# Kernel optimization log

Measured on AMD Instinct MI355X. Metric: run time of the kernel, lower is better.

The kernel has to match this reference:

```python
import jax, jax.numpy as jnp
import numpy as np

HEADS = 16
DIM_HEAD = 32
WSZ = 7
DIM = 512
INNER = HEADS * DIM_HEAD
LN_EPS = 1e-5


def setup_inputs() -> dict:
    key = jax.random.key(0)
    ks = jax.random.split(key, 9)
    b, H, W = 16, 56, 56
    x = jax.random.normal(ks[0], (b, DIM, H, W), dtype=jnp.float32)
    w_qkv = jax.random.normal(ks[1], (INNER * 3, DIM), dtype=jnp.float32) * (DIM ** -0.5)
    window_tokens = jax.random.normal(ks[2], (DIM,), dtype=jnp.float32)
    ln_w = jnp.ones((DIM_HEAD,), dtype=jnp.float32)
    ln_b = jnp.zeros((DIM_HEAD,), dtype=jnp.float32)
    w_qk = jax.random.normal(ks[3], (INNER * 2, INNER), dtype=jnp.float32) * (INNER ** -0.5)
    b_qk = jnp.zeros((INNER * 2,), dtype=jnp.float32)
    w_out = jax.random.normal(ks[4], (DIM, INNER), dtype=jnp.float32) * (INNER ** -0.5)
    b_out = jnp.zeros((DIM,), dtype=jnp.float32)
    return {"x": x, "w_qkv": w_qkv, "window_tokens": window_tokens,
            "ln_w": ln_w, "ln_b": ln_b, "w_qk": w_qk, "b_qk": b_qk,
            "w_out": w_out, "b_out": b_out}


def reference(x, w_qkv, window_tokens, ln_w, ln_b, w_qk, b_qk, w_out, b_out):
    b, c, H, W = x.shape
    h, d, wsz = HEADS, DIM_HEAD, WSZ
    X, Y = H // wsz, W // wsz
    nw = X * Y            # number of windows per image
    n = wsz * wsz         # tokens per window (49)
    scale = d ** -0.5

    # b c (X w1) (Y w2) -> (b X Y) c (w1 w2)
    xw = x.reshape(b, c, X, wsz, Y, wsz).transpose(0, 2, 4, 1, 3, 5).reshape(b * nw, c, n)
    wt = jnp.broadcast_to(window_tokens[None, :, None], (b * nw, c, 1))
    xc = jnp.concatenate([wt, xw], axis=-1)                 # [BW, c, n+1]

    qkv = jnp.einsum('oc,bcn->bon', w_qkv, xc)              # 1x1 conv, no bias
    q, k, v = jnp.split(qkv, 3, axis=1)
    def to_heads(t):
        return t.reshape(t.shape[0], h, d, n + 1).transpose(0, 1, 3, 2)  # [BW,h,n+1,d]
    q, k, v = to_heads(q), to_heads(k), to_heads(v)

    dots = jnp.einsum('bhid,bhjd->bhij', q * scale, k)      # [BW,h,50,50]
    attn = jax.nn.softmax(dots, axis=-1)
    out = jnp.einsum('bhij,bhjd->bhid', attn, v)            # [BW,h,50,d]

    wtok = out[:, :, 0].reshape(b, nw, h, d).transpose(0, 2, 1, 3)          # [b,h,nw,d]
    wfm = out[:, :, 1:].reshape(b, nw, h, n, d).transpose(0, 2, 1, 3, 4)    # [b,h,nw,n,d]

    # window_tokens_to_qk: LayerNorm(d) -> GELU -> conv1d(inner, 2*inner)
    mu = wtok.mean(-1, keepdims=True)
    var = wtok.var(-1, keepdims=True)
    normed = (wtok - mu) / jnp.sqrt(var + LN_EPS) * ln_w + ln_b
    g = jax.nn.gelu(normed, approximate=False)
    gf = g.transpose(0, 1, 3, 2).reshape(b, h * d, nw)      # b h n c -> b (h c) n
    qk = jnp.einsum('oc,bcn->bon', w_qk, gf) + b_qk[None, :, None]
    qk = qk.reshape(b, h, 2 * d, nw).transpose(0, 1, 3, 2)  # [b,h,nw,2d]
    w_q, w_k = qk[..., :d], qk[..., d:]

    w_dots = jnp.einsum('bhid,bhjd->bhij', w_q * scale, w_k)  # [b,h,nw,nw]
    w_attn = jax.nn.softmax(w_dots, axis=-1)
    agg = jnp.einsum('bhij,bhjnd->bhind', w_attn, wfm)        # [b,h,nw,n,d]

    # b h (X Y) (w1 w2) d -> b (h d) (X w1) (Y w2)
    fmap = agg.reshape(b, h, X, Y, wsz, wsz, d).transpose(0, 1, 6, 2, 4, 3, 5).reshape(b, h * d, H, W)
    return jnp.einsum('oc,bchw->bohw', w_out, fmap) + b_out[None, :, None, None]
```

## Files before the change

### kernel.cpp

```cpp
#include <hip/hip_runtime.h>
#include <math.h>

#define SCALE_D 0.17677669529663687f

typedef __attribute__((ext_vector_type(8))) short short8;
typedef __attribute__((ext_vector_type(4))) float f32x4;

__device__ __forceinline__ unsigned short f2bf(float f) {
  unsigned u = __builtin_bit_cast(unsigned, f);
  unsigned r = u + 0x7FFF + ((u >> 16) & 1);
  return (unsigned short)(r >> 16);
}
__device__ __forceinline__ float bf2f(unsigned short h) {
  unsigned u = ((unsigned)h) << 16;
  return __builtin_bit_cast(float, u);
}
__device__ __forceinline__ void gload16(const void* g, void* l) {
  __builtin_amdgcn_global_load_lds((const __attribute__((address_space(1))) unsigned int*)g,
                                   (__attribute__((address_space(3))) unsigned int*)l,
                                   16, 0, 0);
}

__global__ __launch_bounds__(256) void k_split(const float* __restrict__ src,
                                               unsigned short* __restrict__ hi,
                                               unsigned short* __restrict__ lo, int n) {
  int i = blockIdx.x * 256 + threadIdx.x;
  if (i < n) {
    float v = src[i];
    unsigned short h = f2bf(v);
    hi[i] = h;
    lo[i] = f2bf(v - bf2f(h));
  }
}

__global__ __launch_bounds__(256) void k_build_xcT(const float* __restrict__ x,
                                                   const float* __restrict__ wtok,
                                                   unsigned short* __restrict__ Thi,
                                                   unsigned short* __restrict__ Tlo,
                                                   int bb0) {
  const int cblk = blockIdx.x;
  const int h    = blockIdx.y;
  const int bbL  = blockIdx.z;
  const int bb   = bb0 + bbL;
  const int tid  = threadIdx.x;
  const int c0   = cblk * 64;
  if (h == 56) {
    for (int e = tid; e < 4096; e += 256) {
      int wl = e >> 6, cl = e & 63;
      float v = wtok[c0 + cl];
      unsigned short hv = f2bf(v);
      long idx = ((long)(bbL * 64 + wl) * 50) * 512 + c0 + cl;
      Thi[idx] = hv;
      Tlo[idx] = f2bf(v - bf2f(hv));
    }
    return;
  }
  __shared__ unsigned short shi[64][57], slo[64][57];
  const int Xw = h / 7, r7 = h % 7;
  for (int e = tid; e < 3584; e += 256) {
    int cl = e / 56, w = e - cl * 56;
    float v = x[((long)(bb * 512 + c0 + cl) * 56 + h) * 56 + w];
    unsigned short hv = f2bf(v);
    shi[cl][w] = hv;
    slo[cl][w] = f2bf(v - bf2f(hv));
  }
  __syncthreads();
  for (int e = tid; e < 3584; e += 256) {
    int row = e >> 6, cl = e & 63;
    int Yw = row / 7, c7 = row - Yw * 7;
    long trow = (long)(bbL * 64 + Xw * 8 + Yw) * 50 + 1 + r7 * 7 + c7;
    Thi[trow * 512 + c0 + cl] = shi[cl][row];
    Tlo[trow * 512 + c0 + cl] = slo[cl][row];
  }
}

template <int PACK>
__global__ __launch_bounds__(256, 2) void k_gemm_mfma(
    const unsigned short* __restrict__ Ahi, const unsigned short* __restrict__ Alo,
    const unsigned short* __restrict__ Bhi, const unsigned short* __restrict__ Blo,
    float* __restrict__ C, const float* __restrict__ bias,
    int NC, int brow_stride, long c_stride) {
  __shared__ unsigned short lds[2][4][128][32];
  const int tid = threadIdx.x;
  const int wv = tid >> 6, lane = tid & 63;

  const int gy = gridDim.y;
  const int nwg = gridDim.x * gy;
  int hw = blockIdx.y * gridDim.x + blockIdx.x;
  int flat;
  {
    int q = nwg >> 3, r = nwg & 7;
    int xcd = hw & 7, k = hw >> 3;
    int start = (xcd < r) ? xcd * (q + 1) : r * (q + 1) + (xcd - r) * q;
    flat = start + k;
  }
  const int bx = flat / gy, by = flat % gy;
  const int m0 = by * 128, n0 = bx * 128;
  const long brow0 = (long)blockIdx.z * brow_stride + n0;
  C += (long)blockIdx.z * c_stride;

  const int wr = wv >> 1, wc = wv & 1;
  const int lr = lane & 15, kb = lane >> 4;
  const int srow = lane >> 2, sju = lane & 3;
  const int sswz = (sju ^ ((srow >> 1) & 3)) * 8;
  const int rswz = (lr >> 1) & 3;

  f32x4 acc[4][4];
#pragma unroll
  for (int i = 0; i < 4; ++i)
#pragma unroll
    for (int j = 0; j < 4; ++j) {
      f32x4 z = {0.f, 0.f, 0.f, 0.f};
      acc[i][j] = z;
    }

  auto STAGE = [&](int buf, int k0) {
#pragma unroll
    for (int it = 0; it < 2; ++it) {
      const int rloc = (wv * 2 + it) * 16;
      const int r = rloc + srow;
      const long ga = (long)(m0 + r) * 512 + k0 + sswz;
      gload16(Ahi + ga, &lds[buf][0][rloc][0]);
      gload16(Alo + ga, &lds[buf][1][rloc][0]);
      const long gb = (brow0 + r) * 512 + k0 + sswz;
      gload16(Bhi + gb, &lds[buf][2][rloc][0]);
      gload16(Blo + gb, &lds[buf][3][rloc][0]);
    }
  };

  STAGE(0, 0);
  int cur = 0;
  for (int t = 0; t < 16; ++t) {
    if (t < 15) STAGE(cur ^ 1, (t + 1) * 32);
    if (t < 15) {
      asm volatile("s_waitcnt vmcnt(8)" ::: "memory");
    } else {
      asm volatile("s_waitcnt vmcnt(0)" ::: "memory");
    }
    __builtin_amdgcn_s_barrier();
    asm volatile("" ::: "memory");
    short8 ah[4], al[4], bh[4], bl[4];
#pragma unroll
    for (int f = 0; f < 4; ++f) {
      int ra = wr * 64 + f * 16 + lr;
      int ca = (kb ^ rswz) * 8;
      ah[f] = *(const short8*)&lds[cur][0][ra][ca];
      al[f] = *(const short8*)&lds[cur][1][ra][ca];
      int rb = wc * 64 + f * 16 + lr;
      bh[f] = *(const short8*)&lds[cur][2][rb][ca];
      bl[f] = *(const short8*)&lds[cur][3][rb][ca];
    }
#pragma unroll
    for (int i = 0; i < 4; ++i)
#pragma unroll
      for (int j = 0; j < 4; ++j) {
        acc[i][j] = __builtin_amdgcn_mfma_f32_16x16x32_bf16(ah[i], bh[j], acc[i][j], 0, 0, 0);
        acc[i][j] = __builtin_amdgcn_mfma_f32_16x16x32_bf16(ah[i], bl[j], acc[i][j], 0, 0, 0);
        acc[i][j] = __builtin_amdgcn_mfma_f32_16x16x32_bf16(al[i], bh[j], acc[i][j], 0, 0, 0);
      }
    asm volatile("s_waitcnt lgkmcnt(0)" ::: "memory");
    __builtin_amdgcn_s_barrier();
    asm volatile("" ::: "memory");
    cur ^= 1;
  }

#pragma unroll
  for (int i = 0; i < 4; ++i)
#pragma unroll
    for (int nf = 0; nf < 4; ++nf) {
      int col = n0 + wc * 64 + nf * 16 + lr;
      if (col < NC) {
#pragma unroll
        for (int j4 = 0; j4 < 4; ++j4) {
          int row = m0 + wr * 64 + i * 16 + kb * 4 + j4;
          float v = acc[i][nf][j4];
          if (PACK) {
            unsigned short h = f2bf(v);
            unsigned short l = f2bf(v - bf2f(h));
            ((unsigned*)C)[(long)row * NC + col] = (unsigned)h | ((unsigned)l << 16);
          } else {
            C[(long)row * NC + col] = v + (bias ? bias[row] : 0.f);
          }
        }
      }
    }
}

__global__ __launch_bounds__(256) void k_attn1_mfma(const unsigned* __restrict__ QKV,
                                                    float* __restrict__ OUT1, int w0) {
  __shared__ unsigned short P[4][16][72];
  const int tid = threadIdx.x;
  const int wv = tid >> 6, lane = tid & 63;
  const int idx = blockIdx.x * 4 + wv;
  const int wl = idx >> 4, h = idx & 15;
  const int lr = lane & 15, kb = lane >> 4;
  const long tb = (long)wl * 50;

  short8 kh[4], kl[4];
#pragma unroll
  for (int jt = 0; jt < 4; ++jt) {
#pragma unroll
    for (int e = 0; e < 8; ++e) {
      unsigned u = QKV[(long)(512 + h * 32 + kb * 8 + e) * 12800 + tb + jt * 16 + lr];
      kh[jt][e] = (short)(u & 0xFFFF);
      kl[jt][e] = (short)(u >> 16);
    }
  }
  short8 vh[2][2], vl[2][2];
#pragma unroll
  for (int ddt = 0; ddt < 2; ++ddt)
#pragma unroll
    for (int ks = 0; ks < 2; ++ks) {
      const long vb = (long)(1024 + h * 32 + ddt * 16 + lr) * 12800 + tb + ks * 32 + kb * 8;
#pragma unroll
      for (int e = 0; e < 8; ++e) {
        int j = ks * 32 + kb * 8 + e;
        unsigned u = (j < 50) ? QKV[vb + e] : 0u;
        vh[ddt][ks][e] = (short)(u & 0xFFFF);
        vl[ddt][ks][e] = (short)(u >> 16);
      }
    }

  const long ob = (long)((w0 + wl) * 16 + h) * 1600;

  for (int it = 0; it < 4; ++it) {
    short8 qh, ql;
#pragma unroll
    for (int e = 0; e < 8; ++e) {
      unsigned u = QKV[(long)(h * 32 + kb * 8 + e) * 12800 + tb + it * 16 + lr];
      qh[e] = (short)(u & 0xFFFF);
      ql[e] = (short)(u >> 16);
    }
    f32x4 s[4];
#pragma unroll
    for (int jt = 0; jt < 4; ++jt) {
      f32x4 z = {0.f, 0.f, 0.f, 0.f};
      s[jt] = z;
      s[jt] = __builtin_amdgcn_mfma_f32_16x16x32_bf16(qh, kh[jt], s[jt], 0, 0, 0);
      s[jt] = __builtin_amdgcn_mfma_f32_16x16x32_bf16(qh, kl[jt], s[jt], 0, 0, 0);
      s[jt] = __builtin_amdgcn_mfma_f32_16x16x32_bf16(ql, kh[jt], s[jt], 0, 0, 0);
#pragma unroll
      for (int r = 0; r < 4; ++r) s[jt][r] *= SCALE_D;
    }
    if (lr >= 2) {
#pragma unroll
      for (int r = 0; r < 4; ++r) s[3][r] = -1e30f;
    }
    float ex[4][4], rinv[4];
#pragma unroll
    for (int r = 0; r < 4; ++r) {
      float m = fmaxf(fmaxf(s[0][r], s[1][r]), fmaxf(s[2][r], s[3][r]));
      m = fmaxf(m, __shfl_xor(m, 1));
      m = fmaxf(m, __shfl_xor(m, 2));
      m = fmaxf(m, __shfl_xor(m, 4));
      m = fmaxf(m, __shfl_xor(m, 8));
      float sm = 0.f;
#pragma unroll
      for (int jt = 0; jt < 4; ++jt) {
        ex[jt][r] = __expf(s[jt][r] - m);
        sm += ex[jt][r];
      }
      sm += __shfl_xor(sm, 1);
      sm += __shfl_xor(sm, 2);
      sm += __shfl_xor(sm, 4);
      sm += __shfl_xor(sm, 8);
      rinv[r] = 1.f / sm;
    }
#pragma unroll
    for (int jt = 0; jt < 4; ++jt)
#pragma unroll
      for (int r = 0; r < 4; ++r)
        P[wv][kb * 4 + r][jt * 16 + lr] = f2bf(ex[jt][r] * rinv[r]);
    short8 pa0 = *(const short8*)&P[wv][lr][kb * 8];
    short8 pa1 = *(const short8*)&P[wv][lr][32 + kb * 8];
    f32x4 o[2];
#pragma unroll
    for (int ddt = 0; ddt < 2; ++ddt) {
      f32x4 z = {0.f, 0.f, 0.f, 0.f};
      o[ddt] = z;
      o[ddt] = __builtin_amdgcn_mfma_f32_16x16x32_bf16(pa0, vh[ddt][0], o[ddt], 0, 0, 0);
      o[ddt] = __builtin_amdgcn_mfma_f32_16x16x32_bf16(pa0, vl[ddt][0], o[ddt], 0, 0, 0);
      o[ddt] = __builtin_amdgcn_mfma_f32_16x16x32_bf16(pa1, vh[ddt][1], o[ddt], 0, 0, 0);
      o[ddt] = __builtin_amdgcn_mfma_f32_16x16x32_bf16(pa1, vl[ddt][1], o[ddt], 0, 0, 0);
    }
#pragma unroll
    for (int ddt = 0; ddt < 2; ++ddt)
#pragma unroll
      for (int r = 0; r < 4; ++r) {
        int i = it * 16 + kb * 4 + r;
        if (i < 50) OUT1[ob + i * 32 + ddt * 16 + lr] = o[ddt][r];
      }
  }
}

__global__ __launch_bounds__(256) void k_gemm(const float* __restrict__ A,
                                              const float* __restrict__ Bg,
                                              float* __restrict__ C,
                                              const float* __restrict__ bias,
                                              int M, int N, int K, long sB, long sC) {
  Bg += (long)blockIdx.z * sB;
  C  += (long)blockIdx.z * sC;
  __shared__ __align__(16) float As[32][132];
  __shared__ __align__(16) float Bs[32][132];
  const int tid = threadIdx.x;
  const int tx = tid & 15, ty = tid >> 4;
  const int m0 = blockIdx.y * 128, n0 = blockIdx.x * 128;

  float acc[8][8];
#pragma unroll
  for (int q = 0; q < 8; ++q)
#pragma unroll
    for (int r = 0; r < 8; ++r) acc[q][r] = 0.f;

  for (int k0 = 0; k0 < K; k0 += 32) {
#pragma unroll
    for (int it = 0; it < 4; ++it) {
      int idx = tid + it * 256;
      int row = idx >> 3, c4 = idx & 7;
      const float4 f = *(const float4*)&A[(long)(m0 + row) * K + k0 + c4 * 4];
      As[c4 * 4 + 0][row] = f.x;
      As[c4 * 4 + 1][row] = f.y;
      As[c4 * 4 + 2][row] = f.z;
      As[c4 * 4 + 3][row] = f.w;
    }
#pragma unroll
    for (int it = 0; it < 4; ++it) {
      int idx = tid + it * 256;
      int row = idx >> 5, c4 = idx & 31;
      int col = n0 + c4 * 4;
      float4 f;
      if (col + 3 < N) {
        f = *(const float4*)&Bg[(long)(k0 + row) * N + col];
      } else {
        f.x = (col + 0 < N) ? Bg[(long)(k0 + row) * N + col + 0] : 0.f;
        f.y = (col + 1 < N) ? Bg[(long)(k0 + row) * N + col + 1] : 0.f;
        f.z = (col + 2 < N) ? Bg[(long)(k0 + row) * N + col + 2] : 0.f;
        f.w = (col + 3 < N) ? Bg[(long)(k0 + row) * N + col + 3] : 0.f;
      }
      *(float4*)&Bs[row][c4 * 4] = f;
    }
    __syncthreads();
#pragma unroll
    for (int kk = 0; kk < 32; ++kk) {
      const float4 a0 = *(const float4*)&As[kk][ty * 8];
      const float4 a1 = *(const float4*)&As[kk][ty * 8 + 4];
      const float4 b0 = *(const float4*)&Bs[kk][tx * 8];
      const float4 b1 = *(const float4*)&Bs[kk][tx * 8 + 4];
      const float am[8] = {a0.x, a0.y, a0.z, a0.w, a1.x, a1.y, a1.z, a1.w};
      const float bn[8] = {b0.x, b0.y, b0.z, b0.w, b1.x, b1.y, b1.z, b1.w};
#pragma unroll
      for (int q = 0; q < 8; ++q)
#pragma unroll
        for (int r = 0; r < 8; ++r) acc[q][r] += am[q] * bn[r];
    }
    __syncthreads();
  }

#pragma unroll
  for (int q = 0; q < 8; ++q) {
    int m = m0 + ty * 8 + q;
    float bv = bias ? bias[m] : 0.f;
#pragma unroll
    for (int half = 0; half < 8; half += 4) {
      int col = n0 + tx * 8 + half;
#pragma unroll
      for (int rr = 0; rr < 4; ++rr)
        if (col + rr < N) C[(long)m * N + col + rr] = acc[q][half + rr] + bv;
    }
  }
}

__global__ __launch_bounds__(256) void k_ln_gelu(const float* __restrict__ OUT1,
                                                 const float* __restrict__ lnw,
                                                 const float* __restrict__ lnb,
                                                 float* __restrict__ G) {
  const int tid = threadIdx.x;
  const int r = blockIdx.x * 8 + (tid >> 5);
  const int l = tid & 31;
  const int bb = r >> 10, hh = (r >> 6) & 15, wp = r & 63;
  float v = OUT1[((long)((bb * 64 + wp) * 16 + hh)) * 1600 + l];
  float s = v, s2 = v * v;
#pragma unroll
  for (int o = 16; o >= 1; o >>= 1) {
    s += __shfl_xor(s, o, 32);
    s2 += __shfl_xor(s2, o, 32);
  }
  float mu = s * (1.f / 32.f);
  float var = s2 * (1.f / 32.f) - mu * mu;
  float xn = (v - mu) * rsqrtf(var + 1e-5f) * lnw[l] + lnb[l];
  float g = 0.5f * xn * (1.f + erff(xn * 0.70710678118654752f));
  G[((long)(bb * 512 + hh * 32 + l)) * 64 + wp] = g;
}

__global__ __launch_bounds__(256) void k_attn2_mfma(const float* __restrict__ QK,
                                                    const float* __restrict__ OUT1,
                                                    float* __restrict__ AGG) {
  const int bh = blockIdx.x;
  const int bb = bh >> 4, hh = bh & 15;
  const int tid = threadIdx.x;
  const int wv = tid >> 6, lane = tid & 63;
  const int lr = lane & 15, kb = lane >> 4;
  const int wr = wv >> 1, wc = wv & 1;

  __shared__ float wqs[64 * 33], wks[64 * 33];
  __shared__ float sd[64 * 65];
  __shared__ float smx[64], ssum[64];
  __shared__ __align__(16) unsigned short PAh[64][72], PAl[64][72];
  __shared__ __align__(16) unsigned short VTh[64][72], VTl[64][72];

  for (int t = tid; t < 2048; t += 256) {
    int dd = t >> 6, i = t & 63;
    wqs[i * 33 + dd] = QK[((long)(bb * 1024 + hh * 64 + dd)) * 64 + i] * SCALE_D;
    wks[i * 33 + dd] = QK[((long)(bb * 1024 + hh * 64 + 32 + dd)) * 64 + i];
  }
  __syncthreads();
  for (int t = tid; t < 4096; t += 256) {
    int i = t >> 6, j = t & 63;
    float s = 0.f;
#pragma unroll
    for (int dd = 0; dd < 32; ++dd) s += wqs[i * 33 + dd] * wks[j * 33 + dd];
    sd[i * 65 + j] = s;
  }
  __syncthreads();
  if (tid < 64) {
    float mx = -1e30f;
    for (int j = 0; j < 64; ++j) mx = fmaxf(mx, sd[tid * 65 + j]);
    float sm = 0.f;
    for (int j = 0; j < 64; ++j) sm += expf(sd[tid * 65 + j] - mx);
    smx[tid] = mx;
    ssum[tid] = 1.f / sm;
  }
  __syncthreads();
  for (int t = tid; t < 4096; t += 256) {
    int i = t >> 6, j = t & 63;
    float p = expf(sd[i * 65 + j] - smx[i]) * ssum[i];
    unsigned short h = f2bf(p);
    PAh[i][j] = h;
    PAl[i][j] = f2bf(p - bf2f(h));
  }
  __syncthreads();

  const int jstart = blockIdx.y * 13;
  const int ntiles = (blockIdx.y == 0) ? 13 : 12;
  const int swp = tid >> 2, sq = tid & 3;
  const long vbase = ((long)((bb * 64 + swp) * 16 + hh)) * 1600 + 32;
  const long abase = (long)bh * 100352;

  for (int tt = 0; tt < ntiles; ++tt) {
    const int jt = jstart + tt;
    const int jd0 = jt * 64;
    const int JT = (jt == 24) ? 32 : 64;
    for (int jj = 0; jj < (JT >> 4); ++jj) {
      const float4 v4 = *(const float4*)&OUT1[vbase + jd0 + jj * 16 + sq * 4];
#pragma unroll
      for (int e = 0; e < 4; ++e) {
        int jl = jj * 16 + sq * 4 + e;
        float v = (e == 0) ? v4.x : (e == 1) ? v4.y : (e == 2) ? v4.z : v4.w;
        unsigned short h = f2bf(v);
        VTh[jl][swp] = h;
        VTl[jl][swp] = f2bf(v - bf2f(h));
      }
    }
    __syncthreads();
#pragma unroll
    for (int mt = 0; mt < 2; ++mt) {
      const int i0 = wr * 32 + mt * 16;
#pragma unroll
      for (int nt = 0; nt < 2; ++nt) {
        const int jl0 = wc * 32 + nt * 16;
        if (jl0 < JT) {
          f32x4 acc = {0.f, 0.f, 0.f, 0.f};
#pragma unroll
          for (int ks = 0; ks < 2; ++ks) {
            const short8 pah = *(const short8*)&PAh[i0 + lr][ks * 32 + kb * 8];
            const short8 pal = *(const short8*)&PAl[i0 + lr][ks * 32 + kb * 8];
            const short8 vth = *(const short8*)&VTh[jl0 + lr][ks * 32 + kb * 8];
            const short8 vtl = *(const short8*)&VTl[jl0 + lr][ks * 32 + kb * 8];
            acc = __builtin_amdgcn_mfma_f32_16x16x32_bf16(pah, vth, acc, 0, 0, 0);
            acc = __builtin_amdgcn_mfma_f32_16x16x32_bf16(pah, vtl, acc, 0, 0, 0);
            acc = __builtin_amdgcn_mfma_f32_16x16x32_bf16(pal, vth, acc, 0, 0, 0);
          }
#pragma unroll
          for (int r = 0; r < 4; ++r)
            AGG[abase + (long)(i0 + kb * 4 + r) * 1568 + jd0 + jl0 + lr] = acc[r];
        }
      }
    }
    __syncthreads();
  }
}

__global__ __launch_bounds__(256) void k_fmap_T(const float* __restrict__ AGG,
                                                unsigned short* __restrict__ Thi,
                                                unsigned short* __restrict__ Tlo) {
  const int wp = blockIdx.x, bb = blockIdx.y;
  const int Xw = wp >> 3, Yw = wp & 7;
  const int c = threadIdx.x * 2;
  const int hh = c >> 5, d0 = c & 31;
  const long abase = ((long)(bb * 16 + hh) * 64 + wp) * 1568;
  for (int j = 0; j < 49; ++j) {
    float v0 = AGG[abase + j * 32 + d0];
    float v1 = AGG[abase + j * 32 + d0 + 1];
    int hw = (Xw * 7 + j / 7) * 56 + Yw * 7 + j % 7;
    long t = ((long)bb * 3200 + hw) * 512 + c;
    unsigned short h0 = f2bf(v0), h1 = f2bf(v1);
    unsigned short l0 = f2bf(v0 - bf2f(h0)), l1 = f2bf(v1 - bf2f(h1));
    *(unsigned*)&Thi[t] = (unsigned)h0 | ((unsigned)h1 << 16);
    *(unsigned*)&Tlo[t] = (unsigned)l0 | ((unsigned)l1 << 16);
  }
}

__global__ __launch_bounds__(256) void k_padzero(unsigned short* __restrict__ Thi,
                                                 unsigned short* __restrict__ Tlo) {
  const int bb = blockIdx.x;
  for (int e = threadIdx.x; e < 32768; e += 256) {
    long idx = ((long)bb * 3200 + 3136) * 512 + e;
    Thi[idx] = 0;
    Tlo[idx] = 0;
  }
}

extern "C" void kernel_launch(void* const* d_in, const int* in_sizes, int n_in,
                              void* d_out, int out_size, void* d_ws, size_t ws_size,
                              hipStream_t stream) {
  const float* x     = (const float*)d_in[0];
  const float* w_qkv = (const float*)d_in[1];
  const float* wt    = (const float*)d_in[2];
  const float* lnw   = (const float*)d_in[3];
  const float* lnb   = (const float*)d_in[4];
  const float* w_qk  = (const float*)d_in[5];
  const float* b_qk  = (const float*)d_in[6];
  const float* w_out = (const float*)d_in[7];
  const float* b_out = (const float*)d_in[8];
  float* out = (float*)d_out;
  float* ws  = (float*)d_ws;

  float* OUT1 = ws;
  float* AUX  = ws + 26214400L;
  unsigned short* XThi = (unsigned short*)(ws + 21233664L);
  unsigned short* XTlo = XThi + 6553600L;
  float* G  = AUX;
  float* QK = AUX + 524288L;
  unsigned short* WOhi = (unsigned short*)AUX;
  unsigned short* WOlo = WOhi + 262144L;
  unsigned short* FThi = (unsigned short*)ws;
  unsigned short* FTlo = FThi + 26214400L;

  unsigned* QKVc = (unsigned*)d_out;
  unsigned short* Whi = (unsigned short*)(out + 19660800L);
  unsigned short* Wlo = Whi + 786432L;
  float* AGG = out;

  k_split<<<3072, 256, 0, stream>>>(w_qkv, Whi, Wlo, 786432);
  for (int c = 0; c < 4; ++c) {
    k_build_xcT<<<dim3(8, 57, 4), 256, 0, stream>>>(x, wt, XThi, XTlo, c * 4);
    k_gemm_mfma<1><<<dim3(100, 12, 1), 256, 0, stream>>>(Whi, Wlo, XThi, XTlo,
                                                         (float*)QKVc, nullptr,
                                                         12800, 0, 0);
    k_attn1_mfma<<<1024, 256, 0, stream>>>(QKVc, OUT1, c * 256);
  }
  k_ln_gelu<<<2048, 256, 0, stream>>>(OUT1, lnw, lnb, G);
  k_gemm<<<dim3(1, 8, 16), 256, 0, stream>>>(w_qk, G, QK, b_qk,
                                             1024, 64, 512, 512L * 64, 1024L * 64);
  k_split<<<1024, 256, 0, stream>>>(w_out, WOhi, WOlo, 262144);
  k_attn2_mfma<<<dim3(256, 2, 1), 256, 0, stream>>>(QK, OUT1, AGG);
  k_fmap_T<<<dim3(64, 16), 256, 0, stream>>>(AGG, FThi, FTlo);
  k_padzero<<<16, 256, 0, stream>>>(FThi, FTlo);
  k_gemm_mfma<0><<<dim3(25, 4, 16), 256, 0, stream>>>(WOhi, WOlo, FThi, FTlo, out,
                                                      b_out, 3136, 3200, 512L * 3136);
}
```

Measured before the change: 788.9 us.

## Load GEMM A operand directly into double-buffered registers, stage only B in LDS

The split-bf16 MFMA GEMM now reads its A tiles (hi and lo) straight from global memory into two alternating register sets. Only the B tiles still go through LDS via global_load_lds. This halves LDS footprint and LDS read traffic per iteration. The loop is unrolled by two so the register buffers can ping-pong, with vmcnt waits adjusted to the new count of outstanding loads. In exchange it adds more VGPRs and direct global loads with per-lane row strides, which may coalesce worse than the staged path and depend on cache hits.

```diff
diff --git a/kernel.cpp b/kernel.cpp
--- a/kernel.cpp
+++ b/kernel.cpp
@@ -80,7 +80,7 @@
     const unsigned short* __restrict__ Bhi, const unsigned short* __restrict__ Blo,
     float* __restrict__ C, const float* __restrict__ bias,
     int NC, int brow_stride, long c_stride) {
-  __shared__ unsigned short lds[2][4][128][32];
+  __shared__ unsigned short lds[2][2][128][32];
   const int tid = threadIdx.x;
   const int wv = tid >> 6, lane = tid & 63;
 
@@ -104,6 +104,7 @@
   const int srow = lane >> 2, sju = lane & 3;
   const int sswz = (sju ^ ((srow >> 1) & 3)) * 8;
   const int rswz = (lr >> 1) & 3;
+  const long arow = (long)(m0 + wr * 64 + lr) * 512 + kb * 8;
 
   f32x4 acc[4][4];
 #pragma unroll
@@ -114,55 +115,85 @@
       acc[i][j] = z;
     }
 
-  auto STAGE = [&](int buf, int k0) {
+  auto STAGE_B = [&](int buf, int k0) {
 #pragma unroll
     for (int it = 0; it < 2; ++it) {
       const int rloc = (wv * 2 + it) * 16;
-      const int r = rloc + srow;
-      const long ga = (long)(m0 + r) * 512 + k0 + sswz;
-      gload16(Ahi + ga, &lds[buf][0][rloc][0]);
-      gload16(Alo + ga, &lds[buf][1][rloc][0]);
-      const long gb = (brow0 + r) * 512 + k0 + sswz;
-      gload16(Bhi + gb, &lds[buf][2][rloc][0]);
-      gload16(Blo + gb, &lds[buf][3][rloc][0]);
+      const long gb = (brow0 + rloc + srow) * 512 + k0 + sswz;
+      gload16(Bhi + gb, &lds[buf][0][rloc][0]);
+      gload16(Blo + gb, &lds[buf][1][rloc][0]);
     }
   };
 
-  STAGE(0, 0);
+  short8 a0h[4], a0l[4], a1h[4], a1l[4];
+#define LOAD_A(dh, dl, k0)                                        \
+  {                                                               \
+    _Pragma("unroll") for (int f = 0; f < 4; ++f) {               \
+      const long ga = arow + f * 16 * 512 + (k0);                 \
+      dh[f] = *(const short8*)&Ahi[ga];                           \
+      dl[f] = *(const short8*)&Alo[ga];                           \
+    }                                                             \
+  }
+
+#define COMPUTE(ah, al)                                                                    \
+  {                                                                                        \
+    short8 bh[4], bl[4];                                                                   \
+    _Pragma("unroll") for (int f = 0; f < 4; ++f) {                                        \
+      int rb = wc * 64 + f * 16 + lr;                                                      \
+      int ca = (kb ^ rswz) * 8;                                                            \
+      bh[f] = *(const short8*)&lds[cur][0][rb][ca];                                        \
+      bl[f] = *(const short8*)&lds[cur][1][rb][ca];                                        \
+    }                                                                                      \
+    _Pragma("unroll") for (int i = 0; i < 4; ++i)                                          \
+        _Pragma("unroll") for (int j = 0; j < 4; ++j) {                                    \
+      acc[i][j] = __builtin_amdgcn_mfma_f32_16x16x32_bf16(ah[i], bh[j], acc[i][j], 0, 0, 0); \
+      acc[i][j] = __builtin_amdgcn_mfma_f32_16x16x32_bf16(ah[i], bl[j], acc[i][j], 0, 0, 0); \
+      acc[i][j] = __builtin_amdgcn_mfma_f32_16x16x32_bf16(al[i], bh[j], acc[i][j], 0, 0, 0); \
+    }                                                                                      \
+  }
+
+  STAGE_B(0, 0);
+  LOAD_A(a0h, a0l, 0);
   int cur = 0;
-  for (int t = 0; t < 16; ++t) {
-    if (t < 15) STAGE(cur ^ 1, (t + 1) * 32);
-    if (t < 15) {
-      asm volatile("s_waitcnt vmcnt(8)" ::: "memory");
-    } else {
-      asm volatile("s_waitcnt vmcnt(0)" ::: "memory");
-    }
-    __builtin_amdgcn_s_barrier();
-    asm volatile("" ::: "memory");
-    short8 ah[4], al[4], bh[4], bl[4];
-#pragma unroll
-    for (int f = 0; f < 4; ++f) {
-      int ra = wr * 64 + f * 16 + lr;
-      int ca = (kb ^ rswz) * 8;
-      ah[f] = *(const short8*)&lds[cur][0][ra][ca];
-      al[f] = *(const short8*)&lds[cur][1][ra][ca];
-      int rb = wc * 64 + f * 16 + lr;
-      bh[f] = *(const short8*)&lds[cur][2][rb][ca];
-      bl[f] = *(const short8*)&lds[cur][3][rb][ca];
-    }
-#pragma unroll
-    for (int i = 0; i < 4; ++i)
-#pragma unroll
-      for (int j = 0; j < 4; ++j) {
-        acc[i][j] = __builtin_amdgcn_mfma_f32_16x16x32_bf16(ah[i], bh[j], acc[i][j], 0, 0, 0);
-        acc[i][j] = __builtin_amdgcn_mfma_f32_16x16x32_bf16(ah[i], bl[j], acc[i][j], 0, 0, 0);
-        acc[i][j] = __builtin_amdgcn_mfma_f32_16x16x32_bf16(al[i], bh[j], acc[i][j], 0, 0, 0);
-      }
-    asm volatile("s_waitcnt lgkmcnt(0)" ::: "memory");
-    __builtin_amdgcn_s_barrier();
-    asm volatile("" ::: "memory");
-    cur ^= 1;
-  }
+#pragma unroll
+  for (int tt = 0; tt < 8; ++tt) {
+    {
+      const int t = 2 * tt;
+      if (t < 15) {
+        STAGE_B(cur ^ 1, (t + 1) * 32);
+        LOAD_A(a1h, a1l, (t + 1) * 32);
+        asm volatile("s_waitcnt vmcnt(12)" ::: "memory");
+      } else {
+        asm volatile("s_waitcnt vmcnt(0)" ::: "memory");
+      }
+      __builtin_amdgcn_s_barrier();
+      asm volatile("" ::: "memory");
+      COMPUTE(a0h, a0l);
+      asm volatile("s_waitcnt lgkmcnt(0)" ::: "memory");
+      __builtin_amdgcn_s_barrier();
+      asm volatile("" ::: "memory");
+      cur ^= 1;
+    }
+    {
+      const int t = 2 * tt + 1;
+      if (t < 15) {
+        STAGE_B(cur ^ 1, (t + 1) * 32);
+        LOAD_A(a0h, a0l, (t + 1) * 32);
+        asm volatile("s_waitcnt vmcnt(12)" ::: "memory");
+      } else {
+        asm volatile("s_waitcnt vmcnt(0)" ::: "memory");
+      }
+      __builtin_amdgcn_s_barrier();
+      asm volatile("" ::: "memory");
+      COMPUTE(a1h, a1l);
+      asm volatile("s_waitcnt lgkmcnt(0)" ::: "memory");
+      __builtin_amdgcn_s_barrier();
+      asm volatile("" ::: "memory");
+      cur ^= 1;
+    }
+  }
+#undef LOAD_A
+#undef COMPUTE
 
 #pragma unroll
   for (int i = 0; i < 4; ++i)
```

Result: slower. 934.3 us (+18.4%).

## Enlarge MFMA GEMM tiles to 256x256 with 8 waves and interleaved staging

Applied to the files above, without the earlier changes.

The split-bf16 MFMA GEMM moves from 128x128 tiles with 4 waves to 256x256 tiles with 8 waves. Each wave now computes a 128x64 sub-tile. Global-to-LDS prefetch of the next K-slice is interleaved with the MFMA sub-steps instead of being issued up front. The aim is more operand reuse per LDS byte and fewer blocks. The costs are 128 KB of LDS per block, a 128-register accumulator that may spill under the 512-thread launch bound, and in the output GEMM a 13x256 column grid whose B-row reads go past the 3200-row padding (only the writes are guarded).

```diff
diff --git a/kernel.cpp b/kernel.cpp
--- a/kernel.cpp
+++ b/kernel.cpp
@@ -75,12 +75,12 @@
 }
 
 template <int PACK>
-__global__ __launch_bounds__(256, 2) void k_gemm_mfma(
+__global__ __launch_bounds__(512, 2) void k_gemm_mfma(
     const unsigned short* __restrict__ Ahi, const unsigned short* __restrict__ Alo,
     const unsigned short* __restrict__ Bhi, const unsigned short* __restrict__ Blo,
     float* __restrict__ C, const float* __restrict__ bias,
     int NC, int brow_stride, long c_stride) {
-  __shared__ unsigned short lds[2][4][128][32];
+  __shared__ unsigned short lds[2][4][256][32];
   const int tid = threadIdx.x;
   const int wv = tid >> 6, lane = tid & 63;
 
@@ -95,85 +95,93 @@
     flat = start + k;
   }
   const int bx = flat / gy, by = flat % gy;
-  const int m0 = by * 128, n0 = bx * 128;
+  const int m0 = by * 256, n0 = bx * 256;
   const long brow0 = (long)blockIdx.z * brow_stride + n0;
   C += (long)blockIdx.z * c_stride;
 
-  const int wr = wv >> 1, wc = wv & 1;
+  const int wr = wv >> 2, wc = wv & 3;
   const int lr = lane & 15, kb = lane >> 4;
   const int srow = lane >> 2, sju = lane & 3;
   const int sswz = (sju ^ ((srow >> 1) & 3)) * 8;
-  const int rswz = (lr >> 1) & 3;
-
-  f32x4 acc[4][4];
-#pragma unroll
-  for (int i = 0; i < 4; ++i)
+  const int ca = (kb ^ ((lr >> 1) & 3)) * 8;
+
+  f32x4 acc[8][4];
+#pragma unroll
+  for (int i = 0; i < 8; ++i)
 #pragma unroll
     for (int j = 0; j < 4; ++j) {
       f32x4 z = {0.f, 0.f, 0.f, 0.f};
       acc[i][j] = z;
     }
 
-  auto STAGE = [&](int buf, int k0) {
-#pragma unroll
-    for (int it = 0; it < 2; ++it) {
-      const int rloc = (wv * 2 + it) * 16;
-      const int r = rloc + srow;
-      const long ga = (long)(m0 + r) * 512 + k0 + sswz;
-      gload16(Ahi + ga, &lds[buf][0][rloc][0]);
-      gload16(Alo + ga, &lds[buf][1][rloc][0]);
-      const long gb = (brow0 + r) * 512 + k0 + sswz;
-      gload16(Bhi + gb, &lds[buf][2][rloc][0]);
-      gload16(Blo + gb, &lds[buf][3][rloc][0]);
-    }
+  auto STAGE4 = [&](int buf, int k0, int it) {
+    const int rloc = wv * 32 + it * 16;
+    const int r = rloc + srow;
+    const long ga = (long)(m0 + r) * 512 + k0 + sswz;
+    gload16(Ahi + ga, &lds[buf][0][rloc][0]);
+    gload16(Alo + ga, &lds[buf][1][rloc][0]);
+    const long gb = (brow0 + r) * 512 + k0 + sswz;
+    gload16(Bhi + gb, &lds[buf][2][rloc][0]);
+    gload16(Blo + gb, &lds[buf][3][rloc][0]);
   };
 
-  STAGE(0, 0);
+  STAGE4(0, 0, 0);
+  STAGE4(0, 0, 1);
+  asm volatile("s_waitcnt vmcnt(0)" ::: "memory");
+  __builtin_amdgcn_s_barrier();
+
   int cur = 0;
   for (int t = 0; t < 16; ++t) {
-    if (t < 15) STAGE(cur ^ 1, (t + 1) * 32);
-    if (t < 15) {
-      asm volatile("s_waitcnt vmcnt(8)" ::: "memory");
-    } else {
-      asm volatile("s_waitcnt vmcnt(0)" ::: "memory");
-    }
+    short8 bh[4], bl[4];
+#pragma unroll
+    for (int q = 0; q < 4; ++q) {
+      if (t < 15 && q < 2) STAGE4(cur ^ 1, (t + 1) * 32, q);
+      if (q == 0) {
+#pragma unroll
+        for (int nt = 0; nt < 4; ++nt) {
+          int rb = wc * 64 + nt * 16 + lr;
+          bh[nt] = *(const short8*)&lds[cur][2][rb][ca];
+          bl[nt] = *(const short8*)&lds[cur][3][rb][ca];
+        }
+      }
+      const int ra0 = wr * 128 + (q * 2 + 0) * 16 + lr;
+      const int ra1 = wr * 128 + (q * 2 + 1) * 16 + lr;
+      const short8 ah0 = *(const short8*)&lds[cur][0][ra0][ca];
+      const short8 al0 = *(const short8*)&lds[cur][1][ra0][ca];
+      const short8 ah1 = *(const short8*)&lds[cur][0][ra1][ca];
+      const short8 al1 = *(const short8*)&lds[cur][1][ra1][ca];
+#pragma unroll
+      for (int nt = 0; nt < 4; ++nt) {
+        acc[q * 2 + 0][nt] =
+            __builtin_amdgcn_mfma_f32_16x16x32_bf16(ah0, bh[nt], acc[q * 2 + 0][nt], 0, 0, 0);
+        acc[q * 2 + 0][nt] =
+            __builtin_amdgcn_mfma_f32_16x16x32_bf16(ah0, bl[nt], acc[q * 2 + 0][nt], 0, 0, 0);
+        acc[q * 2 + 0][nt] =
+            __builtin_amdgcn_mfma_f32_16x16x32_bf16(al0, bh[nt], acc[q * 2 + 0][nt], 0, 0, 0);
+        acc[q * 2 + 1][nt] =
+            __builtin_amdgcn_mfma_f32_16x16x32_bf16(ah1, bh[nt], acc[q * 2 + 1][nt], 0, 0, 0);
+        acc[q * 2 + 1][nt] =
+            __builtin_amdgcn_mfma_f32_16x16x32_bf16(ah1, bl[nt], acc[q * 2 + 1][nt], 0, 0, 0);
+        acc[q * 2 + 1][nt] =
+            __builtin_amdgcn_mfma_f32_16x16x32_bf16(al1, bh[nt], acc[q * 2 + 1][nt], 0, 0, 0);
+      }
+    }
+    __builtin_amdgcn_sched_barrier(0);
+    asm volatile("s_waitcnt lgkmcnt(0) vmcnt(0)" ::: "memory");
     __builtin_amdgcn_s_barrier();
-    asm volatile("" ::: "memory");
-    short8 ah[4], al[4], bh[4], bl[4];
-#pragma unroll
-    for (int f = 0; f < 4; ++f) {
-      int ra = wr * 64 + f * 16 + lr;
-      int ca = (kb ^ rswz) * 8;
-      ah[f] = *(const short8*)&lds[cur][0][ra][ca];
-      al[f] = *(const short8*)&lds[cur][1][ra][ca];
-      int rb = wc * 64 + f * 16 + lr;
-      bh[f] = *(const short8*)&lds[cur][2][rb][ca];
-      bl[f] = *(const short8*)&lds[cur][3][rb][ca];
-    }
-#pragma unroll
-    for (int i = 0; i < 4; ++i)
-#pragma unroll
-      for (int j = 0; j < 4; ++j) {
-        acc[i][j] = __builtin_amdgcn_mfma_f32_16x16x32_bf16(ah[i], bh[j], acc[i][j], 0, 0, 0);
-        acc[i][j] = __builtin_amdgcn_mfma_f32_16x16x32_bf16(ah[i], bl[j], acc[i][j], 0, 0, 0);
-        acc[i][j] = __builtin_amdgcn_mfma_f32_16x16x32_bf16(al[i], bh[j], acc[i][j], 0, 0, 0);
-      }
-    asm volatile("s_waitcnt lgkmcnt(0)" ::: "memory");
-    __builtin_amdgcn_s_barrier();
-    asm volatile("" ::: "memory");
     cur ^= 1;
   }
 
 #pragma unroll
-  for (int i = 0; i < 4; ++i)
-#pragma unroll
-    for (int nf = 0; nf < 4; ++nf) {
-      int col = n0 + wc * 64 + nf * 16 + lr;
+  for (int mt = 0; mt < 8; ++mt)
+#pragma unroll
+    for (int nt = 0; nt < 4; ++nt) {
+      int col = n0 + wc * 64 + nt * 16 + lr;
       if (col < NC) {
 #pragma unroll
         for (int j4 = 0; j4 < 4; ++j4) {
-          int row = m0 + wr * 64 + i * 16 + kb * 4 + j4;
-          float v = acc[i][nf][j4];
+          int row = m0 + wr * 128 + mt * 16 + kb * 4 + j4;
+          float v = acc[mt][nt][j4];
           if (PACK) {
             unsigned short h = f2bf(v);
             unsigned short l = f2bf(v - bf2f(h));
@@ -554,9 +562,9 @@
   k_split<<<3072, 256, 0, stream>>>(w_qkv, Whi, Wlo, 786432);
   for (int c = 0; c < 4; ++c) {
     k_build_xcT<<<dim3(8, 57, 4), 256, 0, stream>>>(x, wt, XThi, XTlo, c * 4);
-    k_gemm_mfma<1><<<dim3(100, 12, 1), 256, 0, stream>>>(Whi, Wlo, XThi, XTlo,
-                                                         (float*)QKVc, nullptr,
-                                                         12800, 0, 0);
+    k_gemm_mfma<1><<<dim3(50, 6, 1), 512, 0, stream>>>(Whi, Wlo, XThi, XTlo,
+                                                       (float*)QKVc, nullptr,
+                                                       12800, 0, 0);
     k_attn1_mfma<<<1024, 256, 0, stream>>>(QKVc, OUT1, c * 256);
   }
   k_ln_gelu<<<2048, 256, 0, stream>>>(OUT1, lnw, lnb, G);
@@ -566,6 +574,6 @@
   k_attn2_mfma<<<dim3(256, 2, 1), 256, 0, stream>>>(QK, OUT1, AGG);
   k_fmap_T<<<dim3(64, 16), 256, 0, stream>>>(AGG, FThi, FTlo);
   k_padzero<<<16, 256, 0, stream>>>(FThi, FTlo);
-  k_gemm_mfma<0><<<dim3(25, 4, 16), 256, 0, stream>>>(WOhi, WOlo, FThi, FTlo, out,
+  k_gemm_mfma<0><<<dim3(13, 2, 16), 512, 0, stream>>>(WOhi, WOlo, FThi, FTlo, out,
                                                       b_out, 3136, 3200, 512L * 3136);
 }
```

Result: slower. 829.5 us (+5.1%).

## Use 256x256 double-buffered MFMA GEMM with XCD remapping for output projection

Applied to the files above, without the earlier changes.

Adds a new 512-thread GEMM kernel for the final output projection. It uses 256x256 tiles, a double-buffered LDS pipeline fed by direct global-to-LDS loads, XCD-aware block remapping and raised wave priority around the MFMA bursts. The older 128x128 split-bf16 GEMM is replaced for this stage. The aim is more data reuse per tile and overlap of loads with compute. In exchange it uses about 128KB of LDS per block, so only one block fits per CU. Its grid of 416 blocks may also leave CUs unevenly loaded, and the padded B tiles read past the 3200-row padding.

```diff
diff --git a/kernel.cpp b/kernel.cpp
--- a/kernel.cpp
+++ b/kernel.cpp
@@ -186,6 +186,124 @@
     }
 }
 
+__global__ __launch_bounds__(512, 2) void k_gemm_mfma8p(
+    const unsigned short* __restrict__ Ahi, const unsigned short* __restrict__ Alo,
+    const unsigned short* __restrict__ Bhi, const unsigned short* __restrict__ Blo,
+    float* __restrict__ C, const float* __restrict__ bias,
+    int NC, int brow_stride, long c_stride) {
+  __shared__ unsigned short lds[2][4][256][32];
+  const int tid = threadIdx.x;
+  const int wv = tid >> 6, lane = tid & 63;
+
+  const int gy = gridDim.y;
+  const int nwg = gridDim.x * gy;
+  int hw = blockIdx.y * gridDim.x + blockIdx.x;
+  int flat;
+  {
+    int q = nwg >> 3, r = nwg & 7;
+    int xcd = hw & 7, k = hw >> 3;
+    int start = (xcd < r) ? xcd * (q + 1) : r * (q + 1) + (xcd - r) * q;
+    flat = start + k;
+  }
+  const int bx = flat / gy, by = flat % gy;
+  const int m0 = by * 256, n0 = bx * 256;
+  const long brow0 = (long)blockIdx.z * brow_stride + n0;
+  C += (long)blockIdx.z * c_stride;
+
+  const int wr = wv >> 2, wc = wv & 3;
+  const int lr = lane & 15, kb = lane >> 4;
+  const int srow = lane >> 2, sju = lane & 3;
+  const int sswz = (sju ^ ((srow >> 1) & 3)) * 8;
+  const int ca = (kb ^ ((lr >> 1) & 3)) * 8;
+
+  f32x4 acc[8][4];
+#pragma unroll
+  for (int i = 0; i < 8; ++i)
+#pragma unroll
+    for (int j = 0; j < 4; ++j) {
+      f32x4 z = {0.f, 0.f, 0.f, 0.f};
+      acc[i][j] = z;
+    }
+
+  auto STAGE4 = [&](int buf, int k0, int it) {
+    const int rloc = wv * 32 + it * 16;
+    const int r = rloc + srow;
+    const long ga = (long)(m0 + r) * 512 + k0 + sswz;
+    gload16(Ahi + ga, &lds[buf][0][rloc][0]);
+    gload16(Alo + ga, &lds[buf][1][rloc][0]);
+    const long gb = (brow0 + r) * 512 + k0 + sswz;
+    gload16(Bhi + gb, &lds[buf][2][rloc][0]);
+    gload16(Blo + gb, &lds[buf][3][rloc][0]);
+  };
+
+  STAGE4(0, 0, 0);
+  STAGE4(0, 0, 1);
+  asm volatile("s_waitcnt vmcnt(0)" ::: "memory");
+  __builtin_amdgcn_s_barrier();
+
+  int cur = 0;
+  for (int t = 0; t < 16; ++t) {
+    short8 bh[4], bl[4];
+#pragma unroll
+    for (int q = 0; q < 4; ++q) {
+      if (t < 15 && q < 2) STAGE4(cur ^ 1, (t + 1) * 32, q);
+      if (q == 0) {
+#pragma unroll
+        for (int nt = 0; nt < 4; ++nt) {
+          int rb = wc * 64 + nt * 16 + lr;
+          bh[nt] = *(const short8*)&lds[cur][2][rb][ca];
+          bl[nt] = *(const short8*)&lds[cur][3][rb][ca];
+        }
+      }
+      const int ra0 = wr * 128 + (q * 2 + 0) * 16 + lr;
+      const int ra1 = wr * 128 + (q * 2 + 1) * 16 + lr;
+      const short8 ah0 = *(const short8*)&lds[cur][0][ra0][ca];
+      const short8 al0 = *(const short8*)&lds[cur][1][ra0][ca];
+      const short8 ah1 = *(const short8*)&lds[cur][0][ra1][ca];
+      const short8 al1 = *(const short8*)&lds[cur][1][ra1][ca];
+      __builtin_amdgcn_sched_barrier(0);
+      __builtin_amdgcn_s_barrier();
+      asm volatile("s_waitcnt lgkmcnt(0)" ::: "memory");
+      __builtin_amdgcn_sched_barrier(0);
+      __builtin_amdgcn_s_setprio(1);
+#pragma unroll
+      for (int nt = 0; nt < 4; ++nt) {
+        acc[q * 2 + 0][nt] =
+            __builtin_amdgcn_mfma_f32_16x16x32_bf16(ah0, bh[nt], acc[q * 2 + 0][nt], 0, 0, 0);
+        acc[q * 2 + 0][nt] =
+            __builtin_amdgcn_mfma_f32_16x16x32_bf16(ah0, bl[nt], acc[q * 2 + 0][nt], 0, 0, 0);
+        acc[q * 2 + 0][nt] =
+            __builtin_amdgcn_mfma_f32_16x16x32_bf16(al0, bh[nt], acc[q * 2 + 0][nt], 0, 0, 0);
+        acc[q * 2 + 1][nt] =
+            __builtin_amdgcn_mfma_f32_16x16x32_bf16(ah1, bh[nt], acc[q * 2 + 1][nt], 0, 0, 0);
+        acc[q * 2 + 1][nt] =
+            __builtin_amdgcn_mfma_f32_16x16x32_bf16(ah1, bl[nt], acc[q * 2 + 1][nt], 0, 0, 0);
+        acc[q * 2 + 1][nt] =
+            __builtin_amdgcn_mfma_f32_16x16x32_bf16(al1, bh[nt], acc[q * 2 + 1][nt], 0, 0, 0);
+      }
+      __builtin_amdgcn_s_setprio(0);
+      __builtin_amdgcn_sched_barrier(0);
+      if (q < 3) __builtin_amdgcn_s_barrier();
+    }
+    __syncthreads();
+    cur ^= 1;
+  }
+
+#pragma unroll
+  for (int mt = 0; mt < 8; ++mt)
+#pragma unroll
+    for (int nt = 0; nt < 4; ++nt) {
+      int col = n0 + wc * 64 + nt * 16 + lr;
+      if (col < NC) {
+#pragma unroll
+        for (int j4 = 0; j4 < 4; ++j4) {
+          int row = m0 + wr * 128 + mt * 16 + kb * 4 + j4;
+          C[(long)row * NC + col] = acc[mt][nt][j4] + (bias ? bias[row] : 0.f);
+        }
+      }
+    }
+}
+
 __global__ __launch_bounds__(256) void k_attn1_mfma(const unsigned* __restrict__ QKV,
                                                     float* __restrict__ OUT1, int w0) {
   __shared__ unsigned short P[4][16][72];
@@ -566,6 +684,6 @@
   k_attn2_mfma<<<dim3(256, 2, 1), 256, 0, stream>>>(QK, OUT1, AGG);
   k_fmap_T<<<dim3(64, 16), 256, 0, stream>>>(AGG, FThi, FTlo);
   k_padzero<<<16, 256, 0, stream>>>(FThi, FTlo);
-  k_gemm_mfma<0><<<dim3(25, 4, 16), 256, 0, stream>>>(WOhi, WOlo, FThi, FTlo, out,
-                                                      b_out, 3136, 3200, 512L * 3136);
-}
+  k_gemm_mfma8p<<<dim3(13, 2, 16), 512, 0, stream>>>(WOhi, WOlo, FThi, FTlo, out,
+                                                     b_out, 3136, 3200, 512L * 3136);
+}
```

Result: no change. 782.6 us (median of 2 runs) (-0.8%).
